# Kernel optimization log

Hardware: AMD Instinct MI355X
Metric: run time of the kernel (lower is better)

## Reference

```python
import jax, jax.numpy as jnp
import numpy as np

B, T, E, VD, H = 1, 4096, 1024, 2048, 8
KD, HD = E // H, VD // H
EPS = 1e-6


def _make_rel_pos():
    # rotary angles: theta_i = 10000^(-2i/KD), repeated for even/odd pairs
    inv = 1.0 / (10000.0 ** (np.arange(0, KD, 2) / KD))
    angle = np.repeat(inv, 2)[None, :] * np.arange(T)[:, None]  # [T, KD]
    sin = jnp.asarray(np.sin(angle), dtype=jnp.float32)
    cos = jnp.asarray(np.cos(angle), dtype=jnp.float32)
    # per-head causal decay mask: gamma_h^(n-m) for n>=m else 0
    gamma = 1.0 - 2.0 ** (-5.0 - np.arange(H))  # [H]
    n = np.arange(T)
    diff = n[:, None] - n[None, :]  # [T, T]
    logg = np.log(gamma)[:, None, None]
    mask = np.where(diff[None] >= 0, np.exp(logg * np.maximum(diff[None], 0)), 0.0)
    return sin, cos, jnp.asarray(mask, dtype=jnp.float32)


def setup_inputs() -> dict:
    key = jax.random.key(0)
    ks = jax.random.split(key, 6)
    sin, cos, inner_mask = _make_rel_pos()
    s = lambda d: 1.0 / np.sqrt(d)
    return {
        "x": jax.random.normal(ks[0], (B, T, E), dtype=jnp.float32),
        "sin": sin,
        "cos": cos,
        "inner_mask": inner_mask,
        "Wq": jax.random.normal(ks[1], (E, E), dtype=jnp.float32) * s(E),
        "Wk": jax.random.normal(ks[2], (E, E), dtype=jnp.float32) * s(E),
        "Wv": jax.random.normal(ks[3], (E, VD), dtype=jnp.float32) * s(E),
        "Wg": jax.random.normal(ks[4], (E, VD), dtype=jnp.float32) * s(E),
        "Wo": jax.random.normal(ks[5], (VD, E), dtype=jnp.float32) * s(VD),
    }


def _rotate_every_two(x):
    x1 = x[..., ::2]
    x2 = x[..., 1::2]
    return jnp.stack((-x2, x1), axis=-1).reshape(x.shape)


def _theta_shift(x, sin, cos):
    return x * cos + _rotate_every_two(x) * sin


def reference(x, sin, cos, inner_mask, Wq, Wk, Wv, Wg, Wo):
    b, t, e = x.shape
    scaling = KD ** (-0.5)
    q = (x @ Wq).reshape(b, t, H, KD).transpose(0, 2, 1, 3)   # [b,h,t,kd]
    k = (x @ Wk * scaling).reshape(b, t, H, KD).transpose(0, 2, 1, 3)
    v = x @ Wv                                                # [b,t,vd]
    g = x @ Wg                                                # [b,t,vd]
    qr = _theta_shift(q, sin, cos)
    kr = _theta_shift(k, sin, cos)
    vr = v.reshape(b, t, H, HD).transpose(0, 2, 1, 3)         # [b,h,t,hd]
    qk = jnp.einsum('bhtd,bhsd->bhts', qr, kr) * inner_mask   # [b,h,t,t]
    denom = jnp.clip(jnp.abs(jax.lax.stop_gradient(qk)).sum(-1, keepdims=True), 1.0, 50000.0)
    qk = qk / denom
    out = jnp.einsum('bhts,bhsd->bhtd', qk, vr)               # [b,h,t,hd]
    out = out.transpose(0, 2, 1, 3)                           # [b,t,h,hd]
    # RMSNorm over head_dim, no affine
    out = out * jax.lax.rsqrt(jnp.mean(out * out, axis=-1, keepdims=True) + EPS)
    out = out.reshape(b, t, H * HD)
    out = jax.nn.silu(g) * out
    return out @ Wo
```

## Files before the change

kernel.cpp:

```cpp
#include <hip/hip_runtime.h>


typedef __attribute__((ext_vector_type(8)))  short  short8;
typedef __attribute__((ext_vector_type(16))) float  floatx16;

__device__ inline unsigned short f2bf(float f){
  unsigned int u = __builtin_bit_cast(unsigned int, f);
  unsigned int r = (u + 0x7fffu + ((u >> 16) & 1u)) >> 16;
  return (unsigned short)r;
}
__device__ inline float bf2f(unsigned short u){
  unsigned int x = ((unsigned int)u) << 16;
  return __builtin_bit_cast(float, x);
}
__device__ inline void async_cp16(const void* g, const void* l){
  __builtin_amdgcn_global_load_lds((const __attribute__((address_space(1))) void*)g,
                                   (__attribute__((address_space(3))) void*)l, 16, 0, 0);
}

struct us4 { unsigned short a,b,c,d; };
__global__ void k_cvt_x(const float* __restrict__ x, unsigned short* __restrict__ xb, int n4){
  int i = blockIdx.x*blockDim.x + threadIdx.x;
  if (i >= n4) return;
  float4 v = ((const float4*)x)[i];
  us4 o = { f2bf(v.x), f2bf(v.y), f2bf(v.z), f2bf(v.w) };
  ((us4*)xb)[i] = o;
}

struct WPrep  { const float* src; unsigned short* dst; int R; int C; int ntile; };
struct WPrepAll { WPrep w[5]; };
__global__ __launch_bounds__(256) void k_prep_w(WPrepAll a){
  __shared__ float tile[64][65];
  int b = blockIdx.x, i = 0;
  while (b >= a.w[i].ntile){ b -= a.w[i].ntile; ++i; }
  const float* src = a.w[i].src; unsigned short* dst = a.w[i].dst;
  int R = a.w[i].R, C = a.w[i].C;
  int tpr = C >> 6;
  int c0 = (b % tpr)*64, r0 = (b / tpr)*64;
  #pragma unroll
  for (int j=0;j<16;++j){
    int idx = j*256 + threadIdx.x; int r = idx>>6, c = idx&63;
    tile[r][c] = src[(size_t)(r0+r)*C + c0 + c];
  }
  __syncthreads();
  #pragma unroll
  for (int j=0;j<16;++j){
    int idx = j*256 + threadIdx.x; int r = idx>>6, c = idx&63;
    dst[(size_t)(c0+r)*R + r0 + c] = f2bf(tile[c][r]);
  }
}

__global__ __launch_bounds__(256) void k_transpose_b2b(const unsigned short* __restrict__ src,
    unsigned short* __restrict__ dst, int R, int C){
  __shared__ unsigned short tile[64][72];
  int c0 = blockIdx.x*64, r0 = blockIdx.y*64;
  #pragma unroll
  for (int i=0;i<16;++i){
    int idx = i*256 + threadIdx.x; int r = idx>>6, c = idx&63;
    tile[r][c] = src[(size_t)(r0+r)*C + c0 + c];
  }
  __syncthreads();
  #pragma unroll
  for (int i=0;i<16;++i){
    int idx = i*256 + threadIdx.x; int r = idx>>6, c = idx&63;
    dst[(size_t)(c0+r)*R + r0 + c] = tile[c][r];
  }
}

template<int MODE>
__global__ __launch_bounds__(256) void k_gemm_bt(
    const unsigned short* __restrict__ A, const unsigned short* __restrict__ BT,
    int M, int N, int K,
    float* __restrict__ out_f32, unsigned short* __restrict__ out_v,
    unsigned short* __restrict__ out_g)
{
  __shared__ __align__(16) short As[128*64];
  __shared__ __align__(16) short Bs[128*64];
  int bn = blockIdx.x*128, bm = blockIdx.y*128;
  int tid = threadIdx.x;
  int w = tid>>6, l = tid&63;
  int wr = w>>1, wc = w&1;
  int lrow = l&31, lhi = l>>5;
  floatx16 acc[2][2];
  #pragma unroll
  for (int a=0;a<2;++a)
    #pragma unroll
    for (int b=0;b<2;++b)
      #pragma unroll
      for (int j=0;j<16;++j) acc[a][b][j]=0.f;

  int kchunk = K / gridDim.z;
  int k_beg = blockIdx.z * kchunk;
  for (int k0=k_beg; k0<k_beg+kchunk; k0+=64){
    __syncthreads();
    #pragma unroll
    for (int i=0;i<4;++i){
      int idx = i*256 + tid; int r = idx>>3, c = idx&7;
      int cs = c ^ (r&7);
      async_cp16((const char*)A  + ((size_t)(bm+r)*K + k0 + cs*8)*2, &As[idx*8]);
      async_cp16((const char*)BT + ((size_t)(bn+r)*K + k0 + cs*8)*2, &Bs[idx*8]);
    }
    __syncthreads();
    #pragma unroll
    for (int kc=0;kc<4;++kc){
      short8 af[2], bf[2];
      #pragma unroll
      for (int tm=0;tm<2;++tm){
        int row = wr*64 + tm*32 + lrow;
        int pos = (2*kc + lhi) ^ (row&7);
        af[tm] = *(const short8*)&As[row*64 + pos*8];
      }
      #pragma unroll
      for (int tn=0;tn<2;++tn){
        int row = wc*64 + tn*32 + lrow;
        int pos = (2*kc + lhi) ^ (row&7);
        bf[tn] = *(const short8*)&Bs[row*64 + pos*8];
      }
      #pragma unroll
      for (int tm=0;tm<2;++tm)
        #pragma unroll
        for (int tn=0;tn<2;++tn)
          acc[tm][tn] = __builtin_amdgcn_mfma_f32_32x32x16_bf16(af[tm], bf[tn], acc[tm][tn], 0,0,0);
    }
  }
  #pragma unroll
  for (int tm=0;tm<2;++tm)
    #pragma unroll
    for (int tn=0;tn<2;++tn)
      #pragma unroll
      for (int r=0;r<16;++r){
        int row = bm + wr*64 + tm*32 + (r&3) + 8*(r>>2) + 4*lhi;
        int col = bn + wc*64 + tn*32 + lrow;
        float v = acc[tm][tn][r];
        if (MODE==0){
          if (col < 2048)      out_f32[(size_t)row*2048 + col] = v;
          else if (col < 4096) out_v[(size_t)row*2048 + (col-2048)] = f2bf(v);
          else                 out_g[(size_t)row*2048 + (col-4096)] = f2bf(v);
        } else {
          float* dst = out_f32 + (size_t)blockIdx.z*((size_t)M*N);
          dst[(size_t)row*N + col] = v;
        }
      }
}

__global__ void k_addout(const float* __restrict__ p0, const float* __restrict__ p1,
                         float* __restrict__ out, int n4){
  int i = blockIdx.x*blockDim.x + threadIdx.x;
  if (i >= n4) return;
  float4 a = ((const float4*)p0)[i];
  float4 b = ((const float4*)p1)[i];
  float4 o = {a.x+b.x, a.y+b.y, a.z+b.z, a.w+b.w};
  ((float4*)out)[i] = o;
}

__global__ void k_rotary(const float* __restrict__ qk, const float* __restrict__ sinp,
                         const float* __restrict__ cosp,
                         unsigned short* __restrict__ qrp, unsigned short* __restrict__ krp)
{
  int tid = blockIdx.x*blockDim.x + threadIdx.x;
  int t = tid >> 10, p = tid & 1023;
  bool isq = p < 512;
  int c = (isq ? p : p - 512)*2;
  int d = c & 127;
  const float* base = qk + (size_t)t*2048 + (isq ? 0 : 1024) + c;
  float f0 = base[0], f1 = base[1];
  float s0 = sinp[t*128 + d],   s1 = sinp[t*128 + d + 1];
  float c0 = cosp[t*128 + d],   c1 = cosp[t*128 + d + 1];
  float r0 = f0*c0 - f1*s0;
  float r1 = f1*c1 + f0*s1;
  if (!isq){ r0 *= 0.08838834764831845f; r1 *= 0.08838834764831845f; }
  unsigned short* dst = (isq ? qrp : krp) + (size_t)t*1024 + c;
  dst[0] = f2bf(r0); dst[1] = f2bf(r1);
}

__global__ __launch_bounds__(256, 2) void k_attn(
    const unsigned short* __restrict__ qr, const unsigned short* __restrict__ kr,
    const unsigned short* __restrict__ vT,
    unsigned short* __restrict__ o_parts, float* __restrict__ den_g)
{
  int gid = blockIdx.x;
  int head = gid & 7;
  int rest = gid >> 3;
  int qt = 63 - (rest >> 2);
  int chunk = rest & 3;
  int tid = threadIdx.x;
  int w = tid>>6, l = tid&63;
  int qh = w>>1, hh = w&1;
  int lrow = l&31, lhi = l>>5;
  int tbase = qt*64 + qh*32;

  float gamma = 1.f - exp2f(-5.f - (float)head);
  float L = log2f(gamma);

  int dmax = (int)(40.0f/(-L));
  int s_start = tbase - dmax; if (s_start < 0) s_start = 0; s_start &= ~31;
  int N = ((tbase - s_start) >> 5) + 1;
  int q4 = (N+3)>>2;
  int t0 = chunk*q4;
  int t1 = t0 + q4; if (t1 > N) t1 = N;

  floatx16 o[4];
  #pragma unroll
  for (int i=0;i<4;++i)
    #pragma unroll
    for (int j=0;j<16;++j) o[i][j]=0.f;
  float den_ = 0.f;

  if (t0 < t1){
    int sb = s_start + t0*32;
    int se = s_start + (t1-1)*32;

    short8 qf[8];
    const unsigned short* qbase = qr + (size_t)(tbase+lrow)*1024 + head*128 + lhi*8;
    #pragma unroll
    for (int kc=0;kc<8;++kc) qf[kc] = *(const short8*)(qbase + kc*16);

    float lanefac = exp2f(L*((float)lrow - 4.0f*(float)lhi));
    float e1[4], e2[4];
    #pragma unroll
    for (int i=0;i<4;++i){ e1[i] = exp2f(-L*(float)i); e2[i] = exp2f(-L*8.0f*(float)i); }

    const unsigned short* kb = kr + head*128 + lhi*8;
    const unsigned short* vb = vT + (size_t)(head*256 + hh*128)*4096 + lhi*8;

#define LOADK(S0, KF) do{ \
    const unsigned short* kp_ = kb + (size_t)((S0)+lrow)*1024; \
    _Pragma("unroll") \
    for (int kc=0;kc<8;++kc) KF[kc] = *(const short8*)(kp_ + kc*16); \
  }while(0)

#define LOADV(S0, VF) do{ \
    const unsigned short* vp_ = vb + (S0); \
    _Pragma("unroll") \
    for (int nt=0;nt<4;++nt){ \
      const unsigned short* vr_ = vp_ + (size_t)(nt*32+lrow)*4096; \
      _Pragma("unroll") \
      for (int kc=0;kc<2;++kc) VF[nt*2+kc] = *(const short8*)(vr_ + kc*16); \
    } \
  }while(0)

#define COMPUTE(S0, KF, VF) do{ \
    floatx16 s_; \
    _Pragma("unroll") for (int j=0;j<16;++j) s_[j]=0.f; \
    __builtin_amdgcn_s_setprio(1); \
    _Pragma("unroll") \
    for (int kc=0;kc<8;++kc) \
      s_ = __builtin_amdgcn_mfma_f32_32x32x16_bf16(KF[kc], qf[kc], s_, 0,0,0); \
    __builtin_amdgcn_s_setprio(0); \
    float tf_ = exp2f(L*(float)(tbase - (S0))) * lanefac; \
    bool diag_ = ((S0) == tbase); \
    float pv_[16]; \
    _Pragma("unroll") \
    for (int r=0;r<16;++r){ \
      float val_ = s_[r]*(tf_*e1[r&3]*e2[r>>2]); \
      if (diag_){ if (lrow < (r&3)+8*(r>>2)+4*lhi) val_ = 0.f; } \
      den_ += fabsf(val_); \
      pv_[r] = val_; \
    } \
    unsigned int w0_,w1_,w2_,w3_,w4_,w5_,w6_,w7_; \
    asm("v_cvt_pk_bf16_f32 %0, %1, %2" : "=v"(w0_) : "v"(pv_[0]),  "v"(pv_[1])); \
    asm("v_cvt_pk_bf16_f32 %0, %1, %2" : "=v"(w1_) : "v"(pv_[2]),  "v"(pv_[3])); \
    asm("v_cvt_pk_bf16_f32 %0, %1, %2" : "=v"(w2_) : "v"(pv_[4]),  "v"(pv_[5])); \
    asm("v_cvt_pk_bf16_f32 %0, %1, %2" : "=v"(w3_) : "v"(pv_[6]),  "v"(pv_[7])); \
    asm("v_cvt_pk_bf16_f32 %0, %1, %2" : "=v"(w4_) : "v"(pv_[8]),  "v"(pv_[9])); \
    asm("v_cvt_pk_bf16_f32 %0, %1, %2" : "=v"(w5_) : "v"(pv_[10]), "v"(pv_[11])); \
    asm("v_cvt_pk_bf16_f32 %0, %1, %2" : "=v"(w6_) : "v"(pv_[12]), "v"(pv_[13])); \
    asm("v_cvt_pk_bf16_f32 %0, %1, %2" : "=v"(w7_) : "v"(pv_[14]), "v"(pv_[15])); \
    asm("v_permlane32_swap_b32 %0, %1" : "+v"(w0_), "+v"(w2_)); \
    asm("v_permlane32_swap_b32 %0, %1" : "+v"(w1_), "+v"(w3_)); \
    asm("v_permlane32_swap_b32 %0, %1" : "+v"(w4_), "+v"(w6_)); \
    asm("v_permlane32_swap_b32 %0, %1" : "+v"(w5_), "+v"(w7_)); \
    union { unsigned int u[4]; short8 s; } pa0_, pa1_; \
    pa0_.u[0]=w0_; pa0_.u[1]=w1_; pa0_.u[2]=w2_; pa0_.u[3]=w3_; \
    pa1_.u[0]=w4_; pa1_.u[1]=w5_; pa1_.u[2]=w6_; pa1_.u[3]=w7_; \
    __builtin_amdgcn_s_setprio(1); \
    _Pragma("unroll") \
    for (int nt=0;nt<4;++nt){ \
      o[nt] = __builtin_amdgcn_mfma_f32_32x32x16_bf16(pa0_.s, VF[nt*2+0], o[nt], 0,0,0); \
      o[nt] = __builtin_amdgcn_mfma_f32_32x32x16_bf16(pa1_.s, VF[nt*2+1], o[nt], 0,0,0); \
    } \
    __builtin_amdgcn_s_setprio(0); \
  }while(0)

    short8 kfA[8], kfB[8];
    LOADK(sb, kfA);
    for (int s0 = sb;; s0 += 64){
      {
        short8 vfA[8];
        LOADV(s0, vfA);
        if (s0 + 32 <= se) LOADK(s0+32, kfB);
        __builtin_amdgcn_sched_barrier(0);
        COMPUTE(s0, kfA, vfA);
      }
      if (s0 + 32 > se) break;
      {
        short8 vfB[8];
        LOADV(s0+32, vfB);
        if (s0 + 64 <= se) LOADK(s0+64, kfA);
        __builtin_amdgcn_sched_barrier(0);
        COMPUTE(s0+32, kfB, vfB);
      }
      if (s0 + 64 > se) break;
    }
#undef LOADK
#undef LOADV
#undef COMPUTE
  }

  if (hh == 0){
    float d = den_ + __shfl_xor(den_, 32, 64);
    if (lhi == 0)
      den_g[((size_t)chunk*4096 + tbase + lrow)*8 + head] = d;
  }

  unsigned short* ob = o_parts + (size_t)chunk*4096*2048;
  #pragma unroll
  for (int nt=0;nt<4;++nt)
    #pragma unroll
    for (int r=0;r<16;++r){
      int row = (r&3)+8*(r>>2)+4*lhi;
      ob[(size_t)(tbase+row)*2048 + head*256 + hh*128 + nt*32 + lrow] = f2bf(o[nt][r]);
    }
}

__global__ __launch_bounds__(256) void k_rmsgate(const unsigned short* __restrict__ o_parts,
    const unsigned short* __restrict__ g_bf, const float* __restrict__ den_g,
    unsigned short* __restrict__ gated)
{
  int t = blockIdx.x;
  int tid = threadIdx.x;
  int head = tid >> 5;
  float den = den_g[(size_t)t*8 + head]
            + den_g[(size_t)( 4096 + t)*8 + head]
            + den_g[(size_t)( 8192 + t)*8 + head]
            + den_g[(size_t)(12288 + t)*8 + head];
  float rs  = 1.0f/fminf(fmaxf(den, 1.0f), 50000.0f);
  size_t base = (size_t)t*2048 + tid*8;
  const size_t CS = (size_t)4096*2048;
  short8 a0 = *(const short8*)(o_parts + base);
  short8 a1 = *(const short8*)(o_parts + CS + base);
  short8 a2 = *(const short8*)(o_parts + 2*CS + base);
  short8 a3 = *(const short8*)(o_parts + 3*CS + base);
  short8 gv = *(const short8*)(g_bf + base);
  float of[8]; float ss = 0.f;
  #pragma unroll
  for (int j=0;j<8;++j){
    of[j] = (bf2f((unsigned short)a0[j]) + bf2f((unsigned short)a1[j])
           + bf2f((unsigned short)a2[j]) + bf2f((unsigned short)a3[j])) * rs;
    ss += of[j]*of[j];
  }
  #pragma unroll
  for (int off=1; off<32; off<<=1) ss += __shfl_xor(ss, off, 64);
  float rms = rsqrtf(ss*(1.0f/256.0f) + 1e-6f);
  short8 outv;
  #pragma unroll
  for (int j=0;j<8;++j){
    float g = bf2f((unsigned short)gv[j]);
    float si = g / (1.0f + expf(-g));
    outv[j] = (short)f2bf(si * of[j] * rms);
  }
  *(short8*)(gated + base) = outv;
}

extern "C" void kernel_launch(void* const* d_in, const int* in_sizes, int n_in,
                              void* d_out, int out_size, void* d_ws, size_t ws_size,
                              hipStream_t stream)
{
  const float* x    = (const float*)d_in[0];
  const float* sinp = (const float*)d_in[1];
  const float* cosp = (const float*)d_in[2];
  const float* Wq = (const float*)d_in[4];
  const float* Wk = (const float*)d_in[5];
  const float* Wv = (const float*)d_in[6];
  const float* Wg = (const float*)d_in[7];
  const float* Wo = (const float*)d_in[8];

  char* ws = (char*)d_ws;
  size_t off = 0;
  auto alloc = [&](size_t bytes)->char*{ char* p = ws + off; off += (bytes + 255) & ~(size_t)255; return p; };
  unsigned short* x_bf   = (unsigned short*)alloc((size_t)4096*1024*2);
  unsigned short* WallT  = (unsigned short*)alloc((size_t)6144*1024*2);
  float*          qk_f32 = (float*)         alloc((size_t)4096*2048*4);
  unsigned short* v_bf   = (unsigned short*)alloc((size_t)4096*2048*2);
  unsigned short* g_bf   = (unsigned short*)alloc((size_t)4096*2048*2);
  unsigned short* vT     = (unsigned short*)alloc((size_t)2048*4096*2);
  unsigned short* WoT    = (unsigned short*)alloc((size_t)1024*2048*2);
  unsigned short* o_parts= (unsigned short*)alloc((size_t)4*4096*2048*2);
  float*          den_g  = (float*)         alloc((size_t)4*4096*8*4);
  float*          p_out2 = (float*)         alloc((size_t)2*4096*1024*4);
  unsigned short* qrp    = x_bf;
  unsigned short* krp    = WallT;
  unsigned short* gated  = x_bf;

  k_cvt_x<<<4096, 256, 0, stream>>>(x, x_bf, 4096*1024/4);
  WPrepAll pa;
  pa.w[0] = { Wq, WallT,                        1024, 1024, 256 };
  pa.w[1] = { Wk, WallT + 1024*1024,            1024, 1024, 256 };
  pa.w[2] = { Wv, WallT + 2048*1024,            1024, 2048, 512 };
  pa.w[3] = { Wg, WallT + (size_t)4096*1024,    1024, 2048, 512 };
  pa.w[4] = { Wo, WoT,                          2048, 1024, 512 };
  k_prep_w<<<2048, 256, 0, stream>>>(pa);

  k_gemm_bt<0><<<dim3(48,32,1), 256, 0, stream>>>(x_bf, WallT, 4096, 6144, 1024, qk_f32, v_bf, g_bf);

  k_rotary<<<16384, 256, 0, stream>>>(qk_f32, sinp, cosp, qrp, krp);

  k_transpose_b2b<<<dim3(32,64), 256, 0, stream>>>(v_bf, vT, 4096, 2048);

  k_attn<<<2048, 256, 0, stream>>>(qrp, krp, vT, o_parts, den_g);

  k_rmsgate<<<4096, 256, 0, stream>>>(o_parts, g_bf, den_g, gated);

  k_gemm_bt<1><<<dim3(8,32,2), 256, 0, stream>>>(gated, WoT, 4096, 1024, 2048,
                                                 p_out2, nullptr, nullptr);
  k_addout<<<4096, 256, 0, stream>>>(p_out2, p_out2 + (size_t)4096*1024,
                                     (float*)d_out, 4096*1024/4);

  (void)in_sizes; (void)n_in; (void)out_size; (void)ws_size;
}
```

Before: 990.0 us.

## Fuse rotary into QKV GEMM epilogue and double-buffer V loads in attention

Applies the rotary embedding and key scaling inside the QKV GEMM epilogue, using a lane shuffle to fetch the pair element, and writes bf16 q/k directly. This removes the fp32 qk intermediate buffer and the separate rotary kernel launch. The attention loop now prefetches V fragments one step ahead, alongside K, with both double-buffered. Bf16 packing is interleaved with the score scaling. Extra live V registers may pressure occupancy, and the epilogue now reads sin/cos tables per element.

```diff
diff --git a/kernel.cpp b/kernel.cpp
--- a/kernel.cpp
+++ b/kernel.cpp
@@ -72,7 +72,9 @@
     const unsigned short* __restrict__ A, const unsigned short* __restrict__ BT,
     int M, int N, int K,
     float* __restrict__ out_f32, unsigned short* __restrict__ out_v,
-    unsigned short* __restrict__ out_g)
+    unsigned short* __restrict__ out_g,
+    unsigned short* __restrict__ out_q, unsigned short* __restrict__ out_k,
+    const float* __restrict__ sinp, const float* __restrict__ cosp)
 {
   __shared__ __align__(16) short As[128*64];
   __shared__ __align__(16) short Bs[128*64];
@@ -133,7 +135,17 @@
         int col = bn + wc*64 + tn*32 + lrow;
         float v = acc[tm][tn][r];
         if (MODE==0){
-          if (col < 2048)      out_f32[(size_t)row*2048 + col] = v;
+          float p = __shfl_xor(v, 1, 64);
+          if (col < 2048){
+            int d = col & 127;
+            float cs = cosp[row*128 + d];
+            float sn = sinp[row*128 + d];
+            float rot = (col & 1) ? (v*cs + p*sn) : (v*cs - p*sn);
+            if (col < 1024)
+              out_q[(size_t)row*1024 + col] = f2bf(rot);
+            else
+              out_k[(size_t)row*1024 + (col-1024)] = f2bf(rot * 0.08838834764831845f);
+          }
           else if (col < 4096) out_v[(size_t)row*2048 + (col-2048)] = f2bf(v);
           else                 out_g[(size_t)row*2048 + (col-4096)] = f2bf(v);
         } else {
@@ -151,26 +163,6 @@
   float4 b = ((const float4*)p1)[i];
   float4 o = {a.x+b.x, a.y+b.y, a.z+b.z, a.w+b.w};
   ((float4*)out)[i] = o;
-}
-
-__global__ void k_rotary(const float* __restrict__ qk, const float* __restrict__ sinp,
-                         const float* __restrict__ cosp,
-                         unsigned short* __restrict__ qrp, unsigned short* __restrict__ krp)
-{
-  int tid = blockIdx.x*blockDim.x + threadIdx.x;
-  int t = tid >> 10, p = tid & 1023;
-  bool isq = p < 512;
-  int c = (isq ? p : p - 512)*2;
-  int d = c & 127;
-  const float* base = qk + (size_t)t*2048 + (isq ? 0 : 1024) + c;
-  float f0 = base[0], f1 = base[1];
-  float s0 = sinp[t*128 + d],   s1 = sinp[t*128 + d + 1];
-  float c0 = cosp[t*128 + d],   c1 = cosp[t*128 + d + 1];
-  float r0 = f0*c0 - f1*s0;
-  float r1 = f1*c1 + f0*s1;
-  if (!isq){ r0 *= 0.08838834764831845f; r1 *= 0.08838834764831845f; }
-  unsigned short* dst = (isq ? qrp : krp) + (size_t)t*1024 + c;
-  dst[0] = f2bf(r0); dst[1] = f2bf(r1);
 }
 
 __global__ __launch_bounds__(256, 2) void k_attn(
@@ -249,30 +241,26 @@
     __builtin_amdgcn_s_setprio(0); \
     float tf_ = exp2f(L*(float)(tbase - (S0))) * lanefac; \
     bool diag_ = ((S0) == tbase); \
-    float pv_[16]; \
+    unsigned int wv_[8]; \
     _Pragma("unroll") \
-    for (int r=0;r<16;++r){ \
-      float val_ = s_[r]*(tf_*e1[r&3]*e2[r>>2]); \
-      if (diag_){ if (lrow < (r&3)+8*(r>>2)+4*lhi) val_ = 0.f; } \
-      den_ += fabsf(val_); \
-      pv_[r] = val_; \
+    for (int rp=0;rp<8;++rp){ \
+      int r0_ = 2*rp, r1_ = 2*rp+1; \
+      float v0_ = s_[r0_]*(tf_*e1[r0_&3]*e2[r0_>>2]); \
+      float v1_ = s_[r1_]*(tf_*e1[r1_&3]*e2[r1_>>2]); \
+      if (diag_){ \
+        if (lrow < (r0_&3)+8*(r0_>>2)+4*lhi) v0_ = 0.f; \
+        if (lrow < (r1_&3)+8*(r1_>>2)+4*lhi) v1_ = 0.f; \
+      } \
+      den_ += fabsf(v0_) + fabsf(v1_); \
+      asm("v_cvt_pk_bf16_f32 %0, %1, %2" : "=v"(wv_[rp]) : "v"(v0_), "v"(v1_)); \
     } \
-    unsigned int w0_,w1_,w2_,w3_,w4_,w5_,w6_,w7_; \
-    asm("v_cvt_pk_bf16_f32 %0, %1, %2" : "=v"(w0_) : "v"(pv_[0]),  "v"(pv_[1])); \
-    asm("v_cvt_pk_bf16_f32 %0, %1, %2" : "=v"(w1_) : "v"(pv_[2]),  "v"(pv_[3])); \
-    asm("v_cvt_pk_bf16_f32 %0, %1, %2" : "=v"(w2_) : "v"(pv_[4]),  "v"(pv_[5])); \
-    asm("v_cvt_pk_bf16_f32 %0, %1, %2" : "=v"(w3_) : "v"(pv_[6]),  "v"(pv_[7])); \
-    asm("v_cvt_pk_bf16_f32 %0, %1, %2" : "=v"(w4_) : "v"(pv_[8]),  "v"(pv_[9])); \
-    asm("v_cvt_pk_bf16_f32 %0, %1, %2" : "=v"(w5_) : "v"(pv_[10]), "v"(pv_[11])); \
-    asm("v_cvt_pk_bf16_f32 %0, %1, %2" : "=v"(w6_) : "v"(pv_[12]), "v"(pv_[13])); \
-    asm("v_cvt_pk_bf16_f32 %0, %1, %2" : "=v"(w7_) : "v"(pv_[14]), "v"(pv_[15])); \
-    asm("v_permlane32_swap_b32 %0, %1" : "+v"(w0_), "+v"(w2_)); \
-    asm("v_permlane32_swap_b32 %0, %1" : "+v"(w1_), "+v"(w3_)); \
-    asm("v_permlane32_swap_b32 %0, %1" : "+v"(w4_), "+v"(w6_)); \
-    asm("v_permlane32_swap_b32 %0, %1" : "+v"(w5_), "+v"(w7_)); \
+    asm("v_permlane32_swap_b32 %0, %1" : "+v"(wv_[0]), "+v"(wv_[2])); \
+    asm("v_permlane32_swap_b32 %0, %1" : "+v"(wv_[1]), "+v"(wv_[3])); \
+    asm("v_permlane32_swap_b32 %0, %1" : "+v"(wv_[4]), "+v"(wv_[6])); \
+    asm("v_permlane32_swap_b32 %0, %1" : "+v"(wv_[5]), "+v"(wv_[7])); \
     union { unsigned int u[4]; short8 s; } pa0_, pa1_; \
-    pa0_.u[0]=w0_; pa0_.u[1]=w1_; pa0_.u[2]=w2_; pa0_.u[3]=w3_; \
-    pa1_.u[0]=w4_; pa1_.u[1]=w5_; pa1_.u[2]=w6_; pa1_.u[3]=w7_; \
+    pa0_.u[0]=wv_[0]; pa0_.u[1]=wv_[1]; pa0_.u[2]=wv_[2]; pa0_.u[3]=wv_[3]; \
+    pa1_.u[0]=wv_[4]; pa1_.u[1]=wv_[5]; pa1_.u[2]=wv_[6]; pa1_.u[3]=wv_[7]; \
     __builtin_amdgcn_s_setprio(1); \
     _Pragma("unroll") \
     for (int nt=0;nt<4;++nt){ \
@@ -282,21 +270,18 @@
     __builtin_amdgcn_s_setprio(0); \
   }while(0)
 
-    short8 kfA[8], kfB[8];
+    short8 kfA[8], kfB[8], vfA[8], vfB[8];
     LOADK(sb, kfA);
+    LOADV(sb, vfA);
     for (int s0 = sb;; s0 += 64){
       {
-        short8 vfA[8];
-        LOADV(s0, vfA);
-        if (s0 + 32 <= se) LOADK(s0+32, kfB);
+        if (s0 + 32 <= se){ LOADK(s0+32, kfB); LOADV(s0+32, vfB); }
         __builtin_amdgcn_sched_barrier(0);
         COMPUTE(s0, kfA, vfA);
       }
       if (s0 + 32 > se) break;
       {
-        short8 vfB[8];
-        LOADV(s0+32, vfB);
-        if (s0 + 64 <= se) LOADK(s0+64, kfA);
+        if (s0 + 64 <= se){ LOADK(s0+64, kfA); LOADV(s0+64, vfA); }
         __builtin_amdgcn_sched_barrier(0);
         COMPUTE(s0+32, kfB, vfB);
       }
@@ -380,7 +365,8 @@
   auto alloc = [&](size_t bytes)->char*{ char* p = ws + off; off += (bytes + 255) & ~(size_t)255; return p; };
   unsigned short* x_bf   = (unsigned short*)alloc((size_t)4096*1024*2);
   unsigned short* WallT  = (unsigned short*)alloc((size_t)6144*1024*2);
-  float*          qk_f32 = (float*)         alloc((size_t)4096*2048*4);
+  unsigned short* qrp    = (unsigned short*)alloc((size_t)4096*1024*2);
+  unsigned short* krp    = (unsigned short*)alloc((size_t)4096*1024*2);
   unsigned short* v_bf   = (unsigned short*)alloc((size_t)4096*2048*2);
   unsigned short* g_bf   = (unsigned short*)alloc((size_t)4096*2048*2);
   unsigned short* vT     = (unsigned short*)alloc((size_t)2048*4096*2);
@@ -388,8 +374,6 @@
   unsigned short* o_parts= (unsigned short*)alloc((size_t)4*4096*2048*2);
   float*          den_g  = (float*)         alloc((size_t)4*4096*8*4);
   float*          p_out2 = (float*)         alloc((size_t)2*4096*1024*4);
-  unsigned short* qrp    = x_bf;
-  unsigned short* krp    = WallT;
   unsigned short* gated  = x_bf;
 
   k_cvt_x<<<4096, 256, 0, stream>>>(x, x_bf, 4096*1024/4);
@@ -401,9 +385,8 @@
   pa.w[4] = { Wo, WoT,                          2048, 1024, 512 };
   k_prep_w<<<2048, 256, 0, stream>>>(pa);
 
-  k_gemm_bt<0><<<dim3(48,32,1), 256, 0, stream>>>(x_bf, WallT, 4096, 6144, 1024, qk_f32, v_bf, g_bf);
-
-  k_rotary<<<16384, 256, 0, stream>>>(qk_f32, sinp, cosp, qrp, krp);
+  k_gemm_bt<0><<<dim3(48,32,1), 256, 0, stream>>>(x_bf, WallT, 4096, 6144, 1024,
+                                                  nullptr, v_bf, g_bf, qrp, krp, sinp, cosp);
 
   k_transpose_b2b<<<dim3(32,64), 256, 0, stream>>>(v_bf, vT, 4096, 2048);
 
@@ -412,7 +395,8 @@
   k_rmsgate<<<4096, 256, 0, stream>>>(o_parts, g_bf, den_g, gated);
 
   k_gemm_bt<1><<<dim3(8,32,2), 256, 0, stream>>>(gated, WoT, 4096, 1024, 2048,
-                                                 p_out2, nullptr, nullptr);
+                                                 p_out2, nullptr, nullptr,
+                                                 nullptr, nullptr, nullptr, nullptr);
   k_addout<<<4096, 256, 0, stream>>>(p_out2, p_out2 + (size_t)4096*1024,
                                      (float*)d_out, 4096*1024/4);
 
```

After: 1.063 ms. +7.4%, slower.
